# Kernel optimization log

Hardware: AMD Instinct MI355X
Metric: run time of the kernel (lower is better)

The kernel has to match this reference:

```python
import jax, jax.numpy as jnp
import numpy as np

WS = 8          # window_size
SHIFT = WS // 2 # shift for 'SW' type
HEADS = 6
HD = 32


def setup_inputs() -> dict:
    key = jax.random.key(0)
    ks = jax.random.split(key, 6)
    return {
        "x": jax.random.normal(ks[0], (4, 256, 256, 192), jnp.float32),
        "w_qkv": jax.random.normal(ks[1], (192, 576), jnp.float32) * 0.02,
        "b_qkv": jax.random.normal(ks[2], (576,), jnp.float32) * 0.02,
        "rel_pos": jax.random.normal(ks[3], (HEADS, 2 * WS - 1, 2 * WS - 1), jnp.float32) * 0.02,
        "w_out": jax.random.normal(ks[4], (192, 192), jnp.float32) * 0.02,
        "b_out": jax.random.normal(ks[5], (192,), jnp.float32) * 0.02,
    }


def reference(x, w_qkv, b_qkv, rel_pos, w_out, b_out):
    b, h, w, c = x.shape
    scale = HD ** (-0.5)
    wa = WS * WS  # window area
    # shifted-window roll
    x = jnp.roll(x, (-SHIFT, -SHIFT), axis=(1, 2))
    hw, ww = h // WS, w // WS
    nw = hw * ww
    # partition into windows: [b, nw, wa, c]
    xw = x.reshape(b, hw, WS, ww, WS, c).transpose(0, 1, 3, 2, 4, 5).reshape(b, nw, wa, c)
    qkv = xw @ w_qkv + b_qkv                       # [b, nw, wa, 3c]
    qkv = qkv.reshape(b, nw, wa, 3, HEADS, HD)
    q = qkv[..., 0, :, :] * scale
    k = qkv[..., 1, :, :]
    v = qkv[..., 2, :, :]
    attn = jnp.einsum('bnqhd,bnkhd->bnhqk', q, k)  # [b, nw, heads, wa, wa]
    # relative position bias
    coords = jnp.stack(jnp.meshgrid(jnp.arange(WS), jnp.arange(WS), indexing='ij')).reshape(2, -1).T  # [wa,2]
    rel = coords[:, None, :] - coords[None, :, :] + WS - 1   # [wa, wa, 2]
    bias = rel_pos[:, rel[..., 0], rel[..., 1]]              # [heads, wa, wa]
    attn = attn + bias[None, None]
    # shift mask (only last window masked, per the module's generate_mask)
    s = WS - SHIFT
    mask = jnp.zeros((nw, wa, wa), bool)
    mask = mask.at[-1, :s, s:].set(True).at[-1, s:, :s].set(True)
    attn = jnp.where(mask[None, :, None], -jnp.inf, attn)
    attn = jax.nn.softmax(attn, axis=-1)
    out = jnp.einsum('bnhqk,bnkhd->bnqhd', attn, v)          # [b, nw, wa, heads, hd]
    out = out.reshape(b, hw, ww, WS, WS, c).transpose(0, 1, 3, 2, 4, 5).reshape(b, h, w, c)
    out = out @ w_out + b_out
    out = jnp.roll(out, (SHIFT, SHIFT), axis=(1, 2))
    return out
```

## Files before the change

### kernel.cpp

```cpp
#include <hip/hip_runtime.h>
#include <hip/hip_bf16.h>

typedef __attribute__((ext_vector_type(8))) short short8;
typedef __attribute__((ext_vector_type(4))) float f32x4;
typedef __attribute__((ext_vector_type(4))) unsigned short u16x4;

#define MFMA(a, b, c) __builtin_amdgcn_mfma_f32_16x16x32_bf16((a), (b), (c), 0, 0, 0)

namespace {
constexpr int IMG = 256;
constexpr int NWIN = 1024;
constexpr float SCALE = 0.17677669529663687f;
constexpr float L2E   = 1.4426950408889634f;
}

__device__ __forceinline__ unsigned short f2bf1(float f) {
    __hip_bfloat16 h = __float2bfloat16(f);
    union { __hip_bfloat16 h; unsigned short u; } v; v.h = h;
    return v.u;
}
__device__ __forceinline__ unsigned pack2(float a, float b) {
    __hip_bfloat162 h = __float22bfloat162_rn(make_float2(a, b));
    union { __hip_bfloat162 h; unsigned u; } v; v.h = h;
    return v.u;
}
__device__ __forceinline__ float bf2f(unsigned short h) {
    union { unsigned u; float f; } v; v.u = ((unsigned)h) << 16;
    return v.f;
}

__global__ __launch_bounds__(256) void to_bf16_T(const float* __restrict__ in,
                                                 unsigned short* __restrict__ out,
                                                 int K, int N, int scale_n, float scale) {
    __shared__ float tile[32][65];
    const int t = threadIdx.x;
    const int nb = blockIdx.x * 64, kb = blockIdx.y * 32;
    const int tn = t & 63, tk = t >> 6;
#pragma unroll
    for (int p = 0; p < 8; ++p)
        tile[p * 4 + tk][tn] = in[(size_t)(kb + p * 4 + tk) * N + nb + tn];
    __syncthreads();
    const int n = t >> 2, kc = (t & 3) * 8;
    const float s = (nb + n) < scale_n ? scale : 1.0f;
    uint4 u;
    u.x = pack2(tile[kc + 0][n] * s, tile[kc + 1][n] * s);
    u.y = pack2(tile[kc + 2][n] * s, tile[kc + 3][n] * s);
    u.z = pack2(tile[kc + 4][n] * s, tile[kc + 5][n] * s);
    u.w = pack2(tile[kc + 6][n] * s, tile[kc + 7][n] * s);
    *(uint4*)(out + (size_t)(nb + n) * K + kb + kc) = u;
}

__global__ __launch_bounds__(256) void build_bias(const float* __restrict__ rel_pos,
                                                  const float* __restrict__ b_qkv,
                                                  unsigned short* __restrict__ bias2,
                                                  float* __restrict__ bq2) {
    const int o = blockIdx.x * 256 + threadIdx.x;
    const int nt = o & 3, l15 = (o >> 2) & 15, q = (o >> 6) & 63, h = o >> 12;
    const int k = 16 * nt + l15;
    const int qy = q >> 3, qx = q & 7, ky = k >> 3, kx = k & 7;
    const float bv = rel_pos[h * 225 + (qy - ky + 7) * 15 + (qx - kx + 7)] * L2E;
    bias2[o] = f2bf1(bv);
    const bool masked = (q < 4) != (k < 4);
    bias2[24576 + o] = masked ? f2bf1(-30000.0f) : f2bf1(bv);
    if (blockIdx.x == 0) {
        for (int i = threadIdx.x; i < 576; i += 256)
            bq2[i] = b_qkv[i] * (i < 192 ? SCALE : 1.0f);
    }
}

__global__ __launch_bounds__(256, 3)
void qkv_attn(const float* __restrict__ x,
              const float* __restrict__ bq2,
              const unsigned short* __restrict__ bias2,
              const unsigned short* __restrict__ wqT,
              unsigned short* __restrict__ oh_ws) {
    __shared__ unsigned short x_s[64][200];
    __shared__ unsigned short qp_s[64][72];
    __shared__ unsigned short kp_s[64][72];
    __shared__ unsigned short vT_s[64][72];

    const int tid = threadIdx.x;
    const int w   = tid >> 6;
    const int l   = tid & 63;
    const int l15 = l & 15, lg = l >> 4;
    const int wing = blockIdx.x;
    const int b   = wing >> 10;
    const int win = wing & (NWIN - 1);
    const int wy  = win >> 5, wx = win & 31;
    const unsigned short* bias_t = bias2 + ((win == NWIN - 1) ? 24576 : 0);

    for (int i = tid; i < 64 * 48; i += 256) {
        const int t = i / 48, c4 = i % 48;
        const int pr = ((wy << 3) + (t >> 3) + 4) & (IMG - 1);
        const int pc = ((wx << 3) + (t & 7) + 4) & (IMG - 1);
        const float4 xv = *reinterpret_cast<const float4*>(
            x + ((size_t)((b * IMG + pr) * IMG + pc)) * 192 + c4 * 4);
        uint2 pk; pk.x = pack2(xv.x, xv.y); pk.y = pack2(xv.z, xv.w);
        *(uint2*)(&x_s[t][c4 * 4]) = pk;
    }
    __syncthreads();

    const int h_loc = w >> 1;
    const int qt0   = 2 * (w & 1);

#pragma unroll 1
    for (int g = 0; g < 3; ++g) {
        f32x4 aq[3][4];
#pragma unroll
        for (int ci = 0; ci < 3; ++ci) {
            const int t = w + 4 * ci;
            const int which = t >> 2, sub = t & 3;
            const int hh = sub >> 1, d0 = (sub & 1) * 16;
            f32x4 c0;
            if (which < 2) {
                const float4 b4 = *reinterpret_cast<const float4*>(
                    bq2 + which * 192 + (2 * g + hh) * 32 + d0 + 4 * lg);
                c0 = f32x4{b4.x, b4.y, b4.z, b4.w};
            } else {
                const float bb = bq2[384 + (2 * g + hh) * 32 + d0 + l15];
                c0 = f32x4{bb, bb, bb, bb};
            }
#pragma unroll
            for (int nt = 0; nt < 4; ++nt) aq[ci][nt] = c0;
        }

#pragma unroll
        for (int ks = 0; ks < 6; ++ks) {
            short8 xf[4];
#pragma unroll
            for (int nt = 0; nt < 4; ++nt)
                xf[nt] = *(const short8*)(&x_s[16 * nt + l15][ks * 32 + lg * 8]);
#pragma unroll
            for (int ci = 0; ci < 3; ++ci) {
                const int t = w + 4 * ci;
                const int which = t >> 2, sub = t & 3;
                const int hh = sub >> 1, d0 = (sub & 1) * 16;
                const int grow = which * 192 + (2 * g + hh) * 32 + d0 + l15;
                const short8 wf = *(const short8*)(wqT + (size_t)grow * 192 + ks * 32 + lg * 8);
                if (which < 2) {
#pragma unroll
                    for (int nt = 0; nt < 4; ++nt) aq[ci][nt] = MFMA(wf, xf[nt], aq[ci][nt]);
                } else {
#pragma unroll
                    for (int nt = 0; nt < 4; ++nt) aq[ci][nt] = MFMA(xf[nt], wf, aq[ci][nt]);
                }
            }
        }
#pragma unroll
        for (int ci = 0; ci < 3; ++ci) {
            const int t = w + 4 * ci;
            const int which = t >> 2, sub = t & 3;
            const int hh = sub >> 1, d0 = (sub & 1) * 16;
            if (which < 2) {
                const int rbase = hh * 32 + d0 + 4 * lg;
#pragma unroll
                for (int nt = 0; nt < 4; ++nt) {
                    const int tok = 16 * nt + l15;
                    uint2 pk;
                    pk.x = pack2(aq[ci][nt][0], aq[ci][nt][1]);
                    pk.y = pack2(aq[ci][nt][2], aq[ci][nt][3]);
                    if (which == 0) *(uint2*)(&qp_s[tok][rbase]) = pk;
                    else            *(uint2*)(&kp_s[tok][rbase]) = pk;
                }
            } else {
                const int dcol = hh * 32 + d0 + l15;
#pragma unroll
                for (int nt = 0; nt < 4; ++nt) {
                    uint2 pk;
                    pk.x = pack2(aq[ci][nt][0], aq[ci][nt][1]);
                    pk.y = pack2(aq[ci][nt][2], aq[ci][nt][3]);
                    *(uint2*)(&vT_s[dcol][16 * nt + 4 * lg]) = pk;
                }
            }
        }
        __syncthreads();

        short8 qf[2], kf[4];
#pragma unroll
        for (int mq = 0; mq < 2; ++mq)
            qf[mq] = *(const short8*)(&qp_s[16 * (qt0 + mq) + l15][h_loc * 32 + lg * 8]);
#pragma unroll
        for (int nt = 0; nt < 4; ++nt)
            kf[nt] = *(const short8*)(&kp_s[16 * nt + l15][h_loc * 32 + lg * 8]);
        f32x4 s[2][4];
        const f32x4 z = {0.f, 0.f, 0.f, 0.f};
#pragma unroll
        for (int mq = 0; mq < 2; ++mq)
#pragma unroll
            for (int nt = 0; nt < 4; ++nt) s[mq][nt] = MFMA(qf[mq], kf[nt], z);
        __syncthreads();

        unsigned short (*p_buf)[72] = (h_loc == 0) ? qp_s : kp_s;
        const int h = 2 * g + h_loc;
#pragma unroll
        for (int mq = 0; mq < 2; ++mq) {
#pragma unroll
            for (int j = 0; j < 4; ++j) {
                const int q = 16 * (qt0 + mq) + 4 * lg + j;
                const u16x4 bb = *(const u16x4*)(bias_t + (((h * 64 + q) * 16 + l15) << 2));
                float e[4], sum = 0.f;
#pragma unroll
                for (int nt = 0; nt < 4; ++nt) {
                    e[nt] = __builtin_exp2f(fmaf(s[mq][nt][j], L2E, bf2f(bb[nt])));
                    sum += e[nt];
                }
                sum += __shfl_xor(sum, 1);
                sum += __shfl_xor(sum, 2);
                sum += __shfl_xor(sum, 4);
                sum += __shfl_xor(sum, 8);
                const float ri = __builtin_amdgcn_rcpf(sum);
#pragma unroll
                for (int nt = 0; nt < 4; ++nt)
                    p_buf[q][16 * nt + l15] = f2bf1(e[nt] * ri);
            }
        }

        f32x4 o[2][2];
#pragma unroll
        for (int dm = 0; dm < 2; ++dm)
#pragma unroll
            for (int qn = 0; qn < 2; ++qn) o[dm][qn] = z;
#pragma unroll
        for (int ks2 = 0; ks2 < 2; ++ks2) {
            short8 pf[2];
#pragma unroll
            for (int qn = 0; qn < 2; ++qn)
                pf[qn] = *(const short8*)(&p_buf[16 * (qt0 + qn) + l15][ks2 * 32 + lg * 8]);
#pragma unroll
            for (int dm = 0; dm < 2; ++dm) {
                const short8 vf = *(const short8*)(&vT_s[h_loc * 32 + 16 * dm + l15][ks2 * 32 + lg * 8]);
#pragma unroll
                for (int qn = 0; qn < 2; ++qn) o[dm][qn] = MFMA(vf, pf[qn], o[dm][qn]);
            }
        }
#pragma unroll
        for (int dm = 0; dm < 2; ++dm)
#pragma unroll
            for (int qn = 0; qn < 2; ++qn) {
                const int tok = 16 * (qt0 + qn) + l15;
                const int c0 = h * 32 + 16 * dm + 4 * lg;
                uint2 pk;
                pk.x = pack2(o[dm][qn][0], o[dm][qn][1]);
                pk.y = pack2(o[dm][qn][2], o[dm][qn][3]);
                *(uint2*)(oh_ws + (size_t)wing * 12288 + tok * 192 + c0) = pk;
            }
        if (g < 2) __syncthreads();
    }
}

__global__ __launch_bounds__(256, 6)
void gemm2_out(const unsigned short* __restrict__ oh_ws,
               const unsigned short* __restrict__ woT,
               const float* __restrict__ b_out,
               float* __restrict__ out) {
    __shared__ unsigned short oh_s[64][200];

    const int tid = threadIdx.x;
    const int w   = tid >> 6;
    const int l   = tid & 63;
    const int l15 = l & 15, lg = l >> 4;
    const int wing = blockIdx.x;
    const int b   = wing >> 10;
    const int win = wing & (NWIN - 1);
    const int wy  = win >> 5, wx = win & 31;

#pragma unroll
    for (int it = 0; it < 6; ++it) {
        const int i = tid + 256 * it;
        const int t = i / 24, c8 = i % 24;
        const uint4 u = *(const uint4*)(oh_ws + (size_t)wing * 12288 + t * 192 + c8 * 8);
        *(uint4*)(&oh_s[t][c8 * 8]) = u;
    }
    __syncthreads();

#pragma unroll
    for (int ci = 0; ci < 3; ++ci) {
        const int oc0 = 16 * (w + 4 * ci);
        const float4 bo = *reinterpret_cast<const float4*>(b_out + oc0 + 4 * lg);
        f32x4 acc[4];
#pragma unroll
        for (int nt = 0; nt < 4; ++nt) acc[nt] = f32x4{bo.x, bo.y, bo.z, bo.w};
#pragma unroll
        for (int ks = 0; ks < 6; ++ks) {
            const short8 af = *(const short8*)(woT + (size_t)(oc0 + l15) * 192 + ks * 32 + lg * 8);
#pragma unroll
            for (int nt = 0; nt < 4; ++nt) {
                const short8 bfr = *(const short8*)(&oh_s[16 * nt + l15][ks * 32 + lg * 8]);
                acc[nt] = MFMA(af, bfr, acc[nt]);
            }
        }
#pragma unroll
        for (int nt = 0; nt < 4; ++nt) {
            const int tok = 16 * nt + l15;
            const int pr = ((wy << 3) + (tok >> 3) + 4) & (IMG - 1);
            const int pc = ((wx << 3) + (tok & 7) + 4) & (IMG - 1);
            float* orow = out + (size_t)((b * IMG + pr) * IMG + pc) * 192;
            *reinterpret_cast<float4*>(orow + oc0 + 4 * lg) =
                make_float4(acc[nt][0], acc[nt][1], acc[nt][2], acc[nt][3]);
        }
    }
}

extern "C" void kernel_launch(void* const* d_in, const int* in_sizes, int n_in,
                              void* d_out, int out_size, void* d_ws, size_t ws_size,
                              hipStream_t stream) {
    (void)in_sizes; (void)n_in; (void)out_size; (void)ws_size;
    const float* x       = (const float*)d_in[0];
    const float* w_qkv   = (const float*)d_in[1];
    const float* b_qkv   = (const float*)d_in[2];
    const float* rel_pos = (const float*)d_in[3];
    const float* w_out   = (const float*)d_in[4];
    const float* b_out   = (const float*)d_in[5];
    float* out = (float*)d_out;

    unsigned short* wqT   = (unsigned short*)d_ws;
    unsigned short* woT   = wqT + 576 * 192;
    unsigned short* bias2 = woT + 192 * 192;
    float*          bq2   = (float*)(bias2 + 2 * 24576);
    unsigned short* oh_ws = (unsigned short*)(bq2 + 576);

    to_bf16_T<<<dim3(9, 6), 256, 0, stream>>>(w_qkv, wqT, 192, 576, 192, SCALE);
    to_bf16_T<<<dim3(3, 6), 256, 0, stream>>>(w_out, woT, 192, 192, 0, 1.0f);
    build_bias<<<dim3(96), 256, 0, stream>>>(rel_pos, b_qkv, bias2, bq2);

    qkv_attn<<<dim3(4 * NWIN), dim3(256), 0, stream>>>(x, bq2, bias2, wqT, oh_ws);
    gemm2_out<<<dim3(4 * NWIN), dim3(256), 0, stream>>>(oh_ws, woT, b_out, out);
}
```

Before: 325.9 us.

## Transpose score MFMA, defer softmax normalization, unroll x load, prioritize QKV MFMAs

Swaps the QK^T MFMA operands so each lane holds a query row's keys along j. The softmax row sum then needs only two cross-lane shuffles, and P can be stored as packed 4-wide bf16 writes. The 1/sum normalization moves to the output epilogue, and the bias table layout is changed to match. The x-tile load loop is fully unrolled with incremental index math to drop the divides, and s_setprio is raised around the QKV GEMM. Unnormalized bf16 probabilities slightly change rounding.

```diff
diff --git a/kernel.cpp b/kernel.cpp
--- a/kernel.cpp
+++ b/kernel.cpp
@@ -52,16 +52,15 @@
 
 __global__ __launch_bounds__(256) void build_bias(const float* __restrict__ rel_pos,
                                                   const float* __restrict__ b_qkv,
-                                                  unsigned short* __restrict__ bias2,
+                                                  unsigned short* __restrict__ bias3,
                                                   float* __restrict__ bq2) {
     const int o = blockIdx.x * 256 + threadIdx.x;
-    const int nt = o & 3, l15 = (o >> 2) & 15, q = (o >> 6) & 63, h = o >> 12;
-    const int k = 16 * nt + l15;
+    const int k = o & 63, q = (o >> 6) & 63, h = o >> 12;
     const int qy = q >> 3, qx = q & 7, ky = k >> 3, kx = k & 7;
     const float bv = rel_pos[h * 225 + (qy - ky + 7) * 15 + (qx - kx + 7)] * L2E;
-    bias2[o] = f2bf1(bv);
+    bias3[o] = f2bf1(bv);
     const bool masked = (q < 4) != (k < 4);
-    bias2[24576 + o] = masked ? f2bf1(-30000.0f) : f2bf1(bv);
+    bias3[24576 + o] = masked ? f2bf1(-30000.0f) : f2bf1(bv);
     if (blockIdx.x == 0) {
         for (int i = threadIdx.x; i < 576; i += 256)
             bq2[i] = b_qkv[i] * (i < 192 ? SCALE : 1.0f);
@@ -71,7 +70,7 @@
 __global__ __launch_bounds__(256, 3)
 void qkv_attn(const float* __restrict__ x,
               const float* __restrict__ bq2,
-              const unsigned short* __restrict__ bias2,
+              const unsigned short* __restrict__ bias3,
               const unsigned short* __restrict__ wqT,
               unsigned short* __restrict__ oh_ws) {
     __shared__ unsigned short x_s[64][200];
@@ -87,16 +86,21 @@
     const int b   = wing >> 10;
     const int win = wing & (NWIN - 1);
     const int wy  = win >> 5, wx = win & 31;
-    const unsigned short* bias_t = bias2 + ((win == NWIN - 1) ? 24576 : 0);
-
-    for (int i = tid; i < 64 * 48; i += 256) {
-        const int t = i / 48, c4 = i % 48;
-        const int pr = ((wy << 3) + (t >> 3) + 4) & (IMG - 1);
-        const int pc = ((wx << 3) + (t & 7) + 4) & (IMG - 1);
-        const float4 xv = *reinterpret_cast<const float4*>(
-            x + ((size_t)((b * IMG + pr) * IMG + pc)) * 192 + c4 * 4);
-        uint2 pk; pk.x = pack2(xv.x, xv.y); pk.y = pack2(xv.z, xv.w);
-        *(uint2*)(&x_s[t][c4 * 4]) = pk;
+    const unsigned short* bias_t = bias3 + ((win == NWIN - 1) ? 24576 : 0);
+
+    {
+        int t = tid / 48, r = tid % 48;
+#pragma unroll
+        for (int it = 0; it < 12; ++it) {
+            const int pr = ((wy << 3) + (t >> 3) + 4) & (IMG - 1);
+            const int pc = ((wx << 3) + (t & 7) + 4) & (IMG - 1);
+            const float4 xv = *reinterpret_cast<const float4*>(
+                x + ((size_t)((b * IMG + pr) * IMG + pc)) * 192 + r * 4);
+            uint2 pk; pk.x = pack2(xv.x, xv.y); pk.y = pack2(xv.z, xv.w);
+            *(uint2*)(&x_s[t][r * 4]) = pk;
+            r += 16; t += 5;
+            if (r >= 48) { r -= 48; t += 1; }
+        }
     }
     __syncthreads();
 
@@ -124,6 +128,7 @@
             for (int nt = 0; nt < 4; ++nt) aq[ci][nt] = c0;
         }
 
+        __builtin_amdgcn_s_setprio(1);
 #pragma unroll
         for (int ks = 0; ks < 6; ++ks) {
             short8 xf[4];
@@ -146,6 +151,8 @@
                 }
             }
         }
+        __builtin_amdgcn_s_setprio(0);
+
 #pragma unroll
         for (int ci = 0; ci < 3; ++ci) {
             const int t = w + 4 * ci;
@@ -187,31 +194,36 @@
 #pragma unroll
         for (int mq = 0; mq < 2; ++mq)
 #pragma unroll
-            for (int nt = 0; nt < 4; ++nt) s[mq][nt] = MFMA(qf[mq], kf[nt], z);
+            for (int nt = 0; nt < 4; ++nt) s[mq][nt] = MFMA(kf[nt], qf[mq], z);
         __syncthreads();
 
         unsigned short (*p_buf)[72] = (h_loc == 0) ? qp_s : kp_s;
         const int h = 2 * g + h_loc;
+        float ri[2];
 #pragma unroll
         for (int mq = 0; mq < 2; ++mq) {
-#pragma unroll
-            for (int j = 0; j < 4; ++j) {
-                const int q = 16 * (qt0 + mq) + 4 * lg + j;
-                const u16x4 bb = *(const u16x4*)(bias_t + (((h * 64 + q) * 16 + l15) << 2));
-                float e[4], sum = 0.f;
-#pragma unroll
-                for (int nt = 0; nt < 4; ++nt) {
-                    e[nt] = __builtin_exp2f(fmaf(s[mq][nt][j], L2E, bf2f(bb[nt])));
-                    sum += e[nt];
+            const int q = 16 * (qt0 + mq) + l15;
+            float e[4][4], sum = 0.f;
+#pragma unroll
+            for (int nt = 0; nt < 4; ++nt) {
+                const u16x4 bb = *(const u16x4*)(bias_t + (h * 64 + q) * 64 + 16 * nt + 4 * lg);
+                float psum = 0.f;
+#pragma unroll
+                for (int j = 0; j < 4; ++j) {
+                    e[nt][j] = __builtin_exp2f(fmaf(s[mq][nt][j], L2E, bf2f(bb[j])));
+                    psum += e[nt][j];
                 }
-                sum += __shfl_xor(sum, 1);
-                sum += __shfl_xor(sum, 2);
-                sum += __shfl_xor(sum, 4);
-                sum += __shfl_xor(sum, 8);
-                const float ri = __builtin_amdgcn_rcpf(sum);
-#pragma unroll
-                for (int nt = 0; nt < 4; ++nt)
-                    p_buf[q][16 * nt + l15] = f2bf1(e[nt] * ri);
+                sum += psum;
+            }
+            sum += __shfl_xor(sum, 16);
+            sum += __shfl_xor(sum, 32);
+            ri[mq] = __builtin_amdgcn_rcpf(sum);
+#pragma unroll
+            for (int nt = 0; nt < 4; ++nt) {
+                uint2 pk;
+                pk.x = pack2(e[nt][0], e[nt][1]);
+                pk.y = pack2(e[nt][2], e[nt][3]);
+                *(uint2*)(&p_buf[q][16 * nt + 4 * lg]) = pk;
             }
         }
 
@@ -239,9 +251,10 @@
             for (int qn = 0; qn < 2; ++qn) {
                 const int tok = 16 * (qt0 + qn) + l15;
                 const int c0 = h * 32 + 16 * dm + 4 * lg;
+                const float rr = ri[qn];
                 uint2 pk;
-                pk.x = pack2(o[dm][qn][0], o[dm][qn][1]);
-                pk.y = pack2(o[dm][qn][2], o[dm][qn][3]);
+                pk.x = pack2(o[dm][qn][0] * rr, o[dm][qn][1] * rr);
+                pk.y = pack2(o[dm][qn][2] * rr, o[dm][qn][3] * rr);
                 *(uint2*)(oh_ws + (size_t)wing * 12288 + tok * 192 + c0) = pk;
             }
         if (g < 2) __syncthreads();
@@ -315,14 +328,14 @@
 
     unsigned short* wqT   = (unsigned short*)d_ws;
     unsigned short* woT   = wqT + 576 * 192;
-    unsigned short* bias2 = woT + 192 * 192;
-    float*          bq2   = (float*)(bias2 + 2 * 24576);
+    unsigned short* bias3 = woT + 192 * 192;
+    float*          bq2   = (float*)(bias3 + 2 * 24576);
     unsigned short* oh_ws = (unsigned short*)(bq2 + 576);
 
     to_bf16_T<<<dim3(9, 6), 256, 0, stream>>>(w_qkv, wqT, 192, 576, 192, SCALE);
     to_bf16_T<<<dim3(3, 6), 256, 0, stream>>>(w_out, woT, 192, 192, 0, 1.0f);
-    build_bias<<<dim3(96), 256, 0, stream>>>(rel_pos, b_qkv, bias2, bq2);
-
-    qkv_attn<<<dim3(4 * NWIN), dim3(256), 0, stream>>>(x, bq2, bias2, wqT, oh_ws);
+    build_bias<<<dim3(96), 256, 0, stream>>>(rel_pos, b_qkv, bias3, bq2);
+
+    qkv_attn<<<dim3(4 * NWIN), dim3(256), 0, stream>>>(x, bq2, bias3, wqT, oh_ws);
     gemm2_out<<<dim3(4 * NWIN), dim3(256), 0, stream>>>(oh_ws, woT, b_out, out);
 }
```

Result: faster. 314.9 us (-3.4%).
